# Performance work log

Measured on AMD Instinct MI355X. Metric: run time of the kernel, lower is better.

The kernel has to match this reference:

```python
import jax, jax.numpy as jnp
import numpy as np

N, C, K = 8192, 512, 64


def setup_inputs() -> dict:
    key = jax.random.key(0)
    k1, k2, k3 = jax.random.split(key, 3)
    return {
        "f_i": jax.random.normal(k1, (N, C), dtype=jnp.float32),
        "f_j": jax.random.normal(k2, (N, C), dtype=jnp.float32),
        "means": jax.random.normal(k3, (K, C), dtype=jnp.float32),
        "scales": jnp.ones((K, C), dtype=jnp.float32),
        "weights": jnp.ones((K,), dtype=jnp.float32),
    }


def _neg_sq_dist(f, means, scales):
    # f: [N, C], means/scales: [K, C] -> [N, K]
    d = (f[:, None, :] - means[None, :, :]) / scales[None, :, :]
    return -jnp.sum(d * d, axis=-1)


def reference(f_i, f_j, means, scales, weights):
    # Original: kernel[n,m,k] = exp(dist_i[n,k] + dist_j[m,k]); out = kernel @ weights.
    # This factors exactly as (exp(dist_i) * w) @ exp(dist_j)^T, avoiding the
    # O(N*N*K) intermediate while computing identical math.
    dist_i = _neg_sq_dist(f_i, means, scales)  # [N, K]
    dist_j = _neg_sq_dist(f_j, means, scales)  # [N, K]
    phi_i = jnp.exp(dist_i) * weights[None, :]  # [N, K]
    phi_j = jnp.exp(dist_j)                      # [N, K]
    return phi_i @ phi_j.T                       # [N, N]
```

## Files before the change

### kernel.cpp

```cpp
#include <hip/hip_runtime.h>
#include <hip/hip_bf16.h>
#include <math.h>

#define NP   8192
#define CD   512
#define KD   64
#define TWON 16384

typedef __attribute__((ext_vector_type(8))) short short8;
typedef __attribute__((ext_vector_type(4))) float f32x4;

__global__ __launch_bounds__(256) void prep_kernel(
    const float* __restrict__ means, const float* __restrict__ scales,
    float* __restrict__ VT, float* __restrict__ cst)
{
    const int k = blockIdx.x;
    const int t = threadIdx.x;
    __shared__ float red[256];
    float local = 0.f;
    for (int c = t; c < CD; c += 256) {
        float m    = means[k * CD + c];
        float s    = scales[k * CD + c];
        float inv  = 1.0f / s;
        float inv2 = inv * inv;
        VT[c * KD + k]        = 2.0f * m * inv2;
        VT[(CD + c) * KD + k] = -inv2;
        local += m * m * inv2;
    }
    red[t] = local;
    __syncthreads();
    for (int off = 128; off > 0; off >>= 1) {
        if (t < off) red[t] += red[t + off];
        __syncthreads();
    }
    if (t == 0) cst[k] = red[0];
}

__global__ __launch_bounds__(256) void phi_kernel(
    const float* __restrict__ f_i, const float* __restrict__ f_j,
    const float* __restrict__ VT, const float* __restrict__ cst,
    const float* __restrict__ weights, __hip_bfloat16* __restrict__ phi)
{
    __shared__ float Us [64 * 68];
    __shared__ float Vs1[64 * 68];
    __shared__ float Vs2[64 * 68];
    const int t  = threadIdx.x;
    const int n0 = blockIdx.x * 64;
    const bool iside = (n0 < NP);
    const float* f = iside ? (f_i + (size_t)n0 * CD)
                           : (f_j + (size_t)(n0 - NP) * CD);

    const int k0 = (t & 7) * 8;
    const int rg = t >> 3;
    float acc[2][8] = {};

    for (int ch = 0; ch < 8; ++ch) {
        const int c0 = ch * 64;
        #pragma unroll
        for (int j = 0; j < 4; ++j) {
            int v   = t + j * 256;
            int row = v >> 4;
            int c4  = (v & 15) * 4;
            *(float4*)&Us[row * 68 + c4] =
                *(const float4*)&f[(size_t)row * CD + c0 + c4];
            *(float4*)&Vs1[row * 68 + c4] =
                *(const float4*)&VT[(size_t)(c0 + row) * KD + c4];
            *(float4*)&Vs2[row * 68 + c4] =
                *(const float4*)&VT[(size_t)(CD + c0 + row) * KD + c4];
        }
        __syncthreads();

        #pragma unroll 8
        for (int cc = 0; cc < 64; ++cc) {
            float a0 = Us[rg * 68 + cc];
            float a1 = Us[(rg + 32) * 68 + cc];
            float s0 = a0 * a0, s1 = a1 * a1;
            float4 b1a = *(const float4*)&Vs1[cc * 68 + k0];
            float4 b1b = *(const float4*)&Vs1[cc * 68 + k0 + 4];
            float4 b2a = *(const float4*)&Vs2[cc * 68 + k0];
            float4 b2b = *(const float4*)&Vs2[cc * 68 + k0 + 4];
            acc[0][0] += a0 * b1a.x + s0 * b2a.x;
            acc[0][1] += a0 * b1a.y + s0 * b2a.y;
            acc[0][2] += a0 * b1a.z + s0 * b2a.z;
            acc[0][3] += a0 * b1a.w + s0 * b2a.w;
            acc[0][4] += a0 * b1b.x + s0 * b2b.x;
            acc[0][5] += a0 * b1b.y + s0 * b2b.y;
            acc[0][6] += a0 * b1b.z + s0 * b2b.z;
            acc[0][7] += a0 * b1b.w + s0 * b2b.w;
            acc[1][0] += a1 * b1a.x + s1 * b2a.x;
            acc[1][1] += a1 * b1a.y + s1 * b2a.y;
            acc[1][2] += a1 * b1a.z + s1 * b2a.z;
            acc[1][3] += a1 * b1a.w + s1 * b2a.w;
            acc[1][4] += a1 * b1b.x + s1 * b2b.x;
            acc[1][5] += a1 * b1b.y + s1 * b2b.y;
            acc[1][6] += a1 * b1b.z + s1 * b2b.z;
            acc[1][7] += a1 * b1b.w + s1 * b2b.w;
        }
        __syncthreads();
    }

    float cs[8], wv[8];
    *(float4*)&cs[0] = *(const float4*)&cst[k0];
    *(float4*)&cs[4] = *(const float4*)&cst[k0 + 4];
    if (iside) {
        *(float4*)&wv[0] = *(const float4*)&weights[k0];
        *(float4*)&wv[4] = *(const float4*)&weights[k0 + 4];
    } else {
        #pragma unroll
        for (int j = 0; j < 8; ++j) wv[j] = 1.0f;
    }
    #pragma unroll
    for (int r = 0; r < 2; ++r) {
        int row = n0 + rg + r * 32;
        union { short8 v; __hip_bfloat16 h[8]; } o;
        #pragma unroll
        for (int j = 0; j < 8; ++j) {
            float ph = expf(acc[r][j] - cs[j]) * wv[j];
            o.h[j] = __float2bfloat16(ph);
        }
        *(short8*)&phi[(size_t)row * KD + k0] = o.v;
    }
}

__global__ __launch_bounds__(256) void gemm_kernel(
    const __hip_bfloat16* __restrict__ phi, float* __restrict__ out)
{
    const int t    = threadIdx.x;
    const int lane = t & 63, wave = t >> 6;
    const int m    = lane & 15, q = lane >> 4;
    const int i0   = blockIdx.y * 128 + (wave & 1) * 64;
    const int j0   = blockIdx.x * 128 + (wave >> 1) * 64;
    const short* phiS = (const short*)phi;

    short8 A[4][2], B[4][2];
    #pragma unroll
    for (int it = 0; it < 4; ++it)
        #pragma unroll
        for (int kh = 0; kh < 2; ++kh) {
            A[it][kh] = *(const short8*)
                &phiS[(size_t)(i0 + it * 16 + m) * KD + kh * 32 + q * 8];
            B[it][kh] = *(const short8*)
                &phiS[(size_t)(NP + j0 + it * 16 + m) * KD + kh * 32 + q * 8];
        }

    f32x4 acc[4][4];
    #pragma unroll
    for (int it = 0; it < 4; ++it)
        #pragma unroll
        for (int jt = 0; jt < 4; ++jt)
            acc[it][jt] = (f32x4){0.f, 0.f, 0.f, 0.f};

    #pragma unroll
    for (int it = 0; it < 4; ++it)
        #pragma unroll
        for (int jt = 0; jt < 4; ++jt) {
            acc[it][jt] = __builtin_amdgcn_mfma_f32_16x16x32_bf16(
                A[it][0], B[jt][0], acc[it][jt], 0, 0, 0);
            acc[it][jt] = __builtin_amdgcn_mfma_f32_16x16x32_bf16(
                A[it][1], B[jt][1], acc[it][jt], 0, 0, 0);
        }

    #pragma unroll
    for (int it = 0; it < 4; ++it)
        #pragma unroll
        for (int r = 0; r < 4; ++r) {
            size_t row = (size_t)(i0 + it * 16 + q * 4 + r);
            #pragma unroll
            for (int jt = 0; jt < 4; ++jt)
                out[row * NP + j0 + jt * 16 + m] = acc[it][jt][r];
        }
}

extern "C" void kernel_launch(void* const* d_in, const int* in_sizes, int n_in,
                              void* d_out, int out_size, void* d_ws, size_t ws_size,
                              hipStream_t stream) {
    const float* f_i     = (const float*)d_in[0];
    const float* f_j     = (const float*)d_in[1];
    const float* means   = (const float*)d_in[2];
    const float* scales  = (const float*)d_in[3];
    const float* weights = (const float*)d_in[4];
    float* out = (float*)d_out;

    float* ws   = (float*)d_ws;
    float* VT   = ws;
    float* cst  = ws + 65536;
    __hip_bfloat16* phi = (__hip_bfloat16*)(ws + 65600);

    prep_kernel<<<64, 256, 0, stream>>>(means, scales, VT, cst);
    phi_kernel<<<256, 256, 0, stream>>>(f_i, f_j, VT, cst, weights, phi);
    gemm_kernel<<<dim3(64, 64), 256, 0, stream>>>(phi, out);
}
```

Baseline: 357.3 us.

## Move phi distance computation to split-bf16 MFMA and vectorize GEMM output stores

The phi kernel's FP32 FMA loop over shared memory is replaced by bf16 MFMA instructions. Each FP32 operand is split into hi and lo bf16 halves, and three MFMAs per product approximate FP32 accuracy. The prep kernel now writes these split weights transposed, and shared-memory staging plus barriers are removed. The GEMM swaps operand roles so each lane holds four consecutive output columns and can write them with a float4 store instead of scalar strided stores. The risk is a small accuracy loss from the three-term bf16 split and more uncoalesced global loads in phi.

```diff
diff --git a/kernel.cpp b/kernel.cpp
--- a/kernel.cpp
+++ b/kernel.cpp
@@ -6,13 +6,20 @@
 #define CD   512
 #define KD   64
 #define TWON 16384
+#define CC   1024
 
 typedef __attribute__((ext_vector_type(8))) short short8;
 typedef __attribute__((ext_vector_type(4))) float f32x4;
 
+__device__ __forceinline__ void split_bf16(float x, __hip_bfloat16& h, __hip_bfloat16& l) {
+    h = __float2bfloat16(x);
+    l = __float2bfloat16(x - __bfloat162float(h));
+}
+
 __global__ __launch_bounds__(256) void prep_kernel(
     const float* __restrict__ means, const float* __restrict__ scales,
-    float* __restrict__ VT, float* __restrict__ cst)
+    __hip_bfloat16* __restrict__ VTT_hi, __hip_bfloat16* __restrict__ VTT_lo,
+    float* __restrict__ cst)
 {
     const int k = blockIdx.x;
     const int t = threadIdx.x;
@@ -23,8 +30,13 @@
         float s    = scales[k * CD + c];
         float inv  = 1.0f / s;
         float inv2 = inv * inv;
-        VT[c * KD + k]        = 2.0f * m * inv2;
-        VT[(CD + c) * KD + k] = -inv2;
+        __hip_bfloat16 h, l;
+        split_bf16(2.0f * m * inv2, h, l);
+        VTT_hi[(size_t)k * CC + c] = h;
+        VTT_lo[(size_t)k * CC + c] = l;
+        split_bf16(-inv2, h, l);
+        VTT_hi[(size_t)k * CC + CD + c] = h;
+        VTT_lo[(size_t)k * CC + CD + c] = l;
         local += m * m * inv2;
     }
     red[t] = local;
@@ -38,137 +50,112 @@
 
 __global__ __launch_bounds__(256) void phi_kernel(
     const float* __restrict__ f_i, const float* __restrict__ f_j,
-    const float* __restrict__ VT, const float* __restrict__ cst,
-    const float* __restrict__ weights, __hip_bfloat16* __restrict__ phi)
+    const __hip_bfloat16* __restrict__ VTT_hi,
+    const __hip_bfloat16* __restrict__ VTT_lo,
+    const float* __restrict__ cst, const float* __restrict__ weights,
+    __hip_bfloat16* __restrict__ phi)
 {
-    __shared__ float Us [64 * 68];
-    __shared__ float Vs1[64 * 68];
-    __shared__ float Vs2[64 * 68];
-    const int t  = threadIdx.x;
-    const int n0 = blockIdx.x * 64;
-    const bool iside = (n0 < NP);
-    const float* f = iside ? (f_i + (size_t)n0 * CD)
-                           : (f_j + (size_t)(n0 - NP) * CD);
+    const int t = threadIdx.x, lane = t & 63, wave = t >> 6;
+    const int q = lane >> 4, m = lane & 15;
+    const int base = blockIdx.x * 64 + wave * 16;
+    const bool iside = (base < NP);
+    const float* frow = iside ? &f_i[(size_t)(base + m) * CD]
+                              : &f_j[(size_t)(base + m - NP) * CD];
+    const short* BH = (const short*)VTT_hi;
+    const short* BL = (const short*)VTT_lo;
 
-    const int k0 = (t & 7) * 8;
-    const int rg = t >> 3;
-    float acc[2][8] = {};
+    f32x4 acc[4];
+    #pragma unroll
+    for (int nt = 0; nt < 4; ++nt) acc[nt] = (f32x4){0.f, 0.f, 0.f, 0.f};
 
-    for (int ch = 0; ch < 8; ++ch) {
-        const int c0 = ch * 64;
+    for (int ch = 0; ch < 16; ++ch) {
+        const int c0 = ch * 32 + q * 8;
+        float4 x0 = *(const float4*)&frow[c0];
+        float4 x1 = *(const float4*)&frow[c0 + 4];
+        float xs[8] = {x0.x, x0.y, x0.z, x0.w, x1.x, x1.y, x1.z, x1.w};
+        union { short8 v; __hip_bfloat16 h[8]; } aLh, aLl, aSh, aSl;
         #pragma unroll
-        for (int j = 0; j < 4; ++j) {
-            int v   = t + j * 256;
-            int row = v >> 4;
-            int c4  = (v & 15) * 4;
-            *(float4*)&Us[row * 68 + c4] =
-                *(const float4*)&f[(size_t)row * CD + c0 + c4];
-            *(float4*)&Vs1[row * 68 + c4] =
-                *(const float4*)&VT[(size_t)(c0 + row) * KD + c4];
-            *(float4*)&Vs2[row * 68 + c4] =
-                *(const float4*)&VT[(size_t)(CD + c0 + row) * KD + c4];
+        for (int j = 0; j < 8; ++j) {
+            __hip_bfloat16 h, l;
+            split_bf16(xs[j], h, l);          aLh.h[j] = h; aLl.h[j] = l;
+            split_bf16(xs[j] * xs[j], h, l);  aSh.h[j] = h; aSl.h[j] = l;
         }
-        __syncthreads();
-
-        #pragma unroll 8
-        for (int cc = 0; cc < 64; ++cc) {
-            float a0 = Us[rg * 68 + cc];
-            float a1 = Us[(rg + 32) * 68 + cc];
-            float s0 = a0 * a0, s1 = a1 * a1;
-            float4 b1a = *(const float4*)&Vs1[cc * 68 + k0];
-            float4 b1b = *(const float4*)&Vs1[cc * 68 + k0 + 4];
-            float4 b2a = *(const float4*)&Vs2[cc * 68 + k0];
-            float4 b2b = *(const float4*)&Vs2[cc * 68 + k0 + 4];
-            acc[0][0] += a0 * b1a.x + s0 * b2a.x;
-            acc[0][1] += a0 * b1a.y + s0 * b2a.y;
-            acc[0][2] += a0 * b1a.z + s0 * b2a.z;
-            acc[0][3] += a0 * b1a.w + s0 * b2a.w;
-            acc[0][4] += a0 * b1b.x + s0 * b2b.x;
-            acc[0][5] += a0 * b1b.y + s0 * b2b.y;
-            acc[0][6] += a0 * b1b.z + s0 * b2b.z;
-            acc[0][7] += a0 * b1b.w + s0 * b2b.w;
-            acc[1][0] += a1 * b1a.x + s1 * b2a.x;
-            acc[1][1] += a1 * b1a.y + s1 * b2a.y;
-            acc[1][2] += a1 * b1a.z + s1 * b2a.z;
-            acc[1][3] += a1 * b1a.w + s1 * b2a.w;
-            acc[1][4] += a1 * b1b.x + s1 * b2b.x;
-            acc[1][5] += a1 * b1b.y + s1 * b2b.y;
-            acc[1][6] += a1 * b1b.z + s1 * b2b.z;
-            acc[1][7] += a1 * b1b.w + s1 * b2b.w;
+        #pragma unroll
+        for (int nt = 0; nt < 4; ++nt) {
+            const size_t boff = (size_t)(nt * 16 + m) * CC + c0;
+            short8 bh0 = *(const short8*)&BH[boff];
+            short8 bl0 = *(const short8*)&BL[boff];
+            short8 bh1 = *(const short8*)&BH[boff + CD];
+            short8 bl1 = *(const short8*)&BL[boff + CD];
+            acc[nt] = __builtin_amdgcn_mfma_f32_16x16x32_bf16(aLh.v, bh0, acc[nt], 0, 0, 0);
+            acc[nt] = __builtin_amdgcn_mfma_f32_16x16x32_bf16(aLh.v, bl0, acc[nt], 0, 0, 0);
+            acc[nt] = __builtin_amdgcn_mfma_f32_16x16x32_bf16(aLl.v, bh0, acc[nt], 0, 0, 0);
+            acc[nt] = __builtin_amdgcn_mfma_f32_16x16x32_bf16(aSh.v, bh1, acc[nt], 0, 0, 0);
+            acc[nt] = __builtin_amdgcn_mfma_f32_16x16x32_bf16(aSh.v, bl1, acc[nt], 0, 0, 0);
+            acc[nt] = __builtin_amdgcn_mfma_f32_16x16x32_bf16(aSl.v, bh1, acc[nt], 0, 0, 0);
         }
-        __syncthreads();
     }
 
-    float cs[8], wv[8];
-    *(float4*)&cs[0] = *(const float4*)&cst[k0];
-    *(float4*)&cs[4] = *(const float4*)&cst[k0 + 4];
-    if (iside) {
-        *(float4*)&wv[0] = *(const float4*)&weights[k0];
-        *(float4*)&wv[4] = *(const float4*)&weights[k0 + 4];
-    } else {
+    #pragma unroll
+    for (int nt = 0; nt < 4; ++nt) {
+        const int kout = nt * 16 + m;
+        const float cs = cst[kout];
+        const float wv = iside ? weights[kout] : 1.0f;
         #pragma unroll
-        for (int j = 0; j < 8; ++j) wv[j] = 1.0f;
-    }
-    #pragma unroll
-    for (int r = 0; r < 2; ++r) {
-        int row = n0 + rg + r * 32;
-        union { short8 v; __hip_bfloat16 h[8]; } o;
-        #pragma unroll
-        for (int j = 0; j < 8; ++j) {
-            float ph = expf(acc[r][j] - cs[j]) * wv[j];
-            o.h[j] = __float2bfloat16(ph);
+        for (int r = 0; r < 4; ++r) {
+            const int row = base + q * 4 + r;
+            float ph = expf(acc[nt][r] - cs) * wv;
+            phi[(size_t)row * KD + kout] = __float2bfloat16(ph);
         }
-        *(short8*)&phi[(size_t)row * KD + k0] = o.v;
     }
 }
 
 __global__ __launch_bounds__(256) void gemm_kernel(
     const __hip_bfloat16* __restrict__ phi, float* __restrict__ out)
 {
-    const int t    = threadIdx.x;
-    const int lane = t & 63, wave = t >> 6;
-    const int m    = lane & 15, q = lane >> 4;
-    const int i0   = blockIdx.y * 128 + (wave & 1) * 64;
-    const int j0   = blockIdx.x * 128 + (wave >> 1) * 64;
+    const int t = threadIdx.x, lane = t & 63, wave = t >> 6;
+    const int q = lane >> 4, m = lane & 15;
+    const int i0 = blockIdx.y * 128 + (wave & 1) * 64;
+    const int j0 = blockIdx.x * 128 + (wave >> 1) * 64;
     const short* phiS = (const short*)phi;
 
-    short8 A[4][2], B[4][2];
+    short8 Aj[4][2], Bi[4][2];
     #pragma unroll
-    for (int it = 0; it < 4; ++it)
+    for (int tt = 0; tt < 4; ++tt)
         #pragma unroll
         for (int kh = 0; kh < 2; ++kh) {
-            A[it][kh] = *(const short8*)
-                &phiS[(size_t)(i0 + it * 16 + m) * KD + kh * 32 + q * 8];
-            B[it][kh] = *(const short8*)
-                &phiS[(size_t)(NP + j0 + it * 16 + m) * KD + kh * 32 + q * 8];
+            Aj[tt][kh] = *(const short8*)
+                &phiS[(size_t)(NP + j0 + tt * 16 + m) * KD + kh * 32 + q * 8];
+            Bi[tt][kh] = *(const short8*)
+                &phiS[(size_t)(i0 + tt * 16 + m) * KD + kh * 32 + q * 8];
         }
 
     f32x4 acc[4][4];
     #pragma unroll
-    for (int it = 0; it < 4; ++it)
+    for (int bt = 0; bt < 4; ++bt)
         #pragma unroll
-        for (int jt = 0; jt < 4; ++jt)
-            acc[it][jt] = (f32x4){0.f, 0.f, 0.f, 0.f};
+        for (int at = 0; at < 4; ++at)
+            acc[bt][at] = (f32x4){0.f, 0.f, 0.f, 0.f};
 
     #pragma unroll
-    for (int it = 0; it < 4; ++it)
+    for (int bt = 0; bt < 4; ++bt)
         #pragma unroll
-        for (int jt = 0; jt < 4; ++jt) {
-            acc[it][jt] = __builtin_amdgcn_mfma_f32_16x16x32_bf16(
-                A[it][0], B[jt][0], acc[it][jt], 0, 0, 0);
-            acc[it][jt] = __builtin_amdgcn_mfma_f32_16x16x32_bf16(
-                A[it][1], B[jt][1], acc[it][jt], 0, 0, 0);
+        for (int at = 0; at < 4; ++at) {
+            acc[bt][at] = __builtin_amdgcn_mfma_f32_16x16x32_bf16(
+                Aj[at][0], Bi[bt][0], acc[bt][at], 0, 0, 0);
+            acc[bt][at] = __builtin_amdgcn_mfma_f32_16x16x32_bf16(
+                Aj[at][1], Bi[bt][1], acc[bt][at], 0, 0, 0);
         }
 
     #pragma unroll
-    for (int it = 0; it < 4; ++it)
+    for (int bt = 0; bt < 4; ++bt) {
+        const size_t row = (size_t)(i0 + bt * 16 + m);
         #pragma unroll
-        for (int r = 0; r < 4; ++r) {
-            size_t row = (size_t)(i0 + it * 16 + q * 4 + r);
-            #pragma unroll
-            for (int jt = 0; jt < 4; ++jt)
-                out[row * NP + j0 + jt * 16 + m] = acc[it][jt][r];
-        }
+        for (int at = 0; at < 4; ++at)
+            *(float4*)&out[row * NP + j0 + at * 16 + q * 4] =
+                (float4){acc[bt][at][0], acc[bt][at][1],
+                         acc[bt][at][2], acc[bt][at][3]};
+    }
 }
 
 extern "C" void kernel_launch(void* const* d_in, const int* in_sizes, int n_in,
@@ -181,12 +168,13 @@
     const float* weights = (const float*)d_in[4];
     float* out = (float*)d_out;
 
-    float* ws   = (float*)d_ws;
-    float* VT   = ws;
-    float* cst  = ws + 65536;
-    __hip_bfloat16* phi = (__hip_bfloat16*)(ws + 65600);
+    char* ws = (char*)d_ws;
+    __hip_bfloat16* VTT_hi = (__hip_bfloat16*)(ws);
+    __hip_bfloat16* VTT_lo = (__hip_bfloat16*)(ws + 131072);
+    float*          cst    = (float*)(ws + 262144);
+    __hip_bfloat16* phi    = (__hip_bfloat16*)(ws + 262400);
 
-    prep_kernel<<<64, 256, 0, stream>>>(means, scales, VT, cst);
-    phi_kernel<<<256, 256, 0, stream>>>(f_i, f_j, VT, cst, weights, phi);
+    prep_kernel<<<64, 256, 0, stream>>>(means, scales, VTT_hi, VTT_lo, cst);
+    phi_kernel<<<256, 256, 0, stream>>>(f_i, f_j, VTT_hi, VTT_lo, cst, weights, phi);
     gemm_kernel<<<dim3(64, 64), 256, 0, stream>>>(phi, out);
 }
```

Result: faster. 336.0 us (-6.0%).
